# Performance work log

Hardware: AMD Instinct MI355X
Metric: run time of the kernel (lower is better)

The kernel has to match this reference:

```python
import jax, jax.numpy as jnp
import numpy as np

DIM = 1024
HEADS = 16
HEAD_DIM = DIM // HEADS


def setup_inputs() -> dict:
    key = jax.random.key(0)
    k1, k2, k3 = jax.random.split(key, 3)
    x = jax.random.normal(k1, (4, 4096, DIM), dtype=jnp.float32)
    # nn.Linear weights; stored as [out, in] in torch, apply as x @ W.T
    w_qkv = jax.random.normal(k2, (3 * DIM, DIM), dtype=jnp.float32) * (1.0 / np.sqrt(DIM))
    w_out = jax.random.normal(k3, (DIM, DIM), dtype=jnp.float32) * (1.0 / np.sqrt(DIM))
    return {"x": x, "w_qkv": w_qkv, "w_out": w_out}


def _feature_map(t):
    # ELU + 1 (always positive)
    return jax.nn.elu(t) + 1.0


def reference(x, w_qkv, w_out):
    b, n, _ = x.shape
    qkv = x @ w_qkv.T  # [b, n, 3*dim]
    q, k, v = jnp.split(qkv, 3, axis=-1)
    # [b, n, dim] -> [b, h, n, d]
    def to_heads(t):
        return t.reshape(b, n, HEADS, HEAD_DIM).transpose(0, 2, 1, 3)
    q, k, v = to_heads(q), to_heads(k), to_heads(v)
    q = _feature_map(q)
    k = _feature_map(k)
    # KV state: [b, h, d, e]
    kv = jnp.einsum('bhnd,bhne->bhde', k, v)
    out = jnp.einsum('bhnd,bhde->bhne', q, kv)  # [b, h, n, e]
    k_sum = k.sum(axis=2)  # [b, h, d]
    normalizer = jnp.einsum('bhnd,bhd->bhn', q, k_sum)  # [b, h, n]
    out = out / (normalizer[..., None] + 1e-06)
    out = out.transpose(0, 2, 1, 3).reshape(b, n, DIM)
    return out @ w_out.T
```

## Files before the change

### kernel.cpp

```cpp
#include <hip/hip_runtime.h>
#include <hip/hip_bf16.h>
#include <stdint.h>

typedef __attribute__((ext_vector_type(8))) short short8;
typedef __attribute__((ext_vector_type(4))) float f32x4;
typedef __attribute__((ext_vector_type(4))) unsigned short ushort4_t;

#define SEG 16

__device__ __forceinline__ float bf2f(unsigned short u) {
  unsigned int x = ((unsigned int)u) << 16;
  return __uint_as_float(x);
}
__device__ __forceinline__ unsigned short f2bf(float f) {
  unsigned int u = __float_as_uint(f);
  u += 0x7fffu + ((u >> 16) & 1u);
  return (unsigned short)(u >> 16);
}

__device__ __forceinline__ void gload16(const unsigned short* g, unsigned short* l) {
  __builtin_amdgcn_global_load_lds(
      (const __attribute__((address_space(1))) void*)g,
      (__attribute__((address_space(3))) void*)l, 16, 0, 0);
}

__global__ void cast_f32_bf16(const float* __restrict__ in,
                              unsigned short* __restrict__ out, int n4) {
  const int stride = gridDim.x * blockDim.x;
  for (int i = blockIdx.x * blockDim.x + threadIdx.x; i < n4; i += stride) {
    const float4 v = ((const float4*)in)[i];
    ushort4_t o;
    o[0] = f2bf(v.x); o[1] = f2bf(v.y); o[2] = f2bf(v.z); o[3] = f2bf(v.w);
    ((ushort4_t*)out)[i] = o;
  }
}

#define MIDBAR() do { __builtin_amdgcn_sched_barrier(0); __builtin_amdgcn_s_barrier(); } while (0)
#define ENDBAR() do { __builtin_amdgcn_s_barrier(); __builtin_amdgcn_sched_barrier(0); } while (0)

template <typename OutT>
__global__ __launch_bounds__(512, 4) void gemm_v3(
    const unsigned short* __restrict__ A, const unsigned short* __restrict__ Bm,
    OutT* __restrict__ C, int M, int N, int K, int ldc, int fm_cols) {
  __shared__ unsigned short lds[2 * 12288];
  const int tid = threadIdx.x;
  const int lane = tid & 63;
  const int w = tid >> 6;
  const int wr = w >> 1, wc = w & 1;
  const int gx = gridDim.x;
  const int nwg = gx * gridDim.y;
  const int hwid = blockIdx.y * gx + blockIdx.x;
  const int cpx = nwg >> 3;
  const int L = (hwid & 7) * cpx + (hwid >> 3);
  const int bx = L % gx, by = L / gx;
  const size_t arow0 = (size_t)by * 256;
  const size_t bcol0 = (size_t)bx * 128;
  const int nt = K >> 5;

  const int rl = lane >> 2;
  const int sce = (((lane & 3) ^ (rl & 3)) << 3);
  const unsigned short* Ab0 = A + (arow0 + w * 16 + rl) * K + sce;
  const unsigned short* Ab1 = A + (arow0 + 128 + w * 16 + rl) * K + sce;
  const unsigned short* Bb0 = Bm + (bcol0 + w * 16 + rl) * K + sce;

  auto stageA0 = [&](int kt, unsigned short* buf) {
    gload16(Ab0 + ((kt < nt ? kt : kt - nt) << 5), buf + w * 512);
  };
  auto stageA1 = [&](int kt, unsigned short* buf) {
    gload16(Ab1 + ((kt < nt ? kt : kt - nt) << 5), buf + 4096 + w * 512);
  };
  auto stageB = [&](int kt, unsigned short* buf) {
    gload16(Bb0 + ((kt < nt ? kt : kt - nt) << 5), buf + 8192 + w * 512);
  };

  f32x4 acc[4][4] = {};
  const int fr = lane & 15;
  const int kc = lane >> 4;

  auto rdA = [&](const unsigned short* buf, int mm) {
    const int r = wr * 64 + mm * 16 + fr;
    return *(const short8*)&buf[r * 32 + ((kc ^ (r & 3)) << 3)];
  };
  auto rdB = [&](const unsigned short* buf, int nn) {
    const int r = wc * 64 + nn * 16 + fr;
    return *(const short8*)&buf[8192 + r * 32 + ((kc ^ (r & 3)) << 3)];
  };

  stageA0(0, lds); stageA1(0, lds); stageB(0, lds);
  asm volatile("s_waitcnt vmcnt(0)" ::: "memory");
  __builtin_amdgcn_s_barrier();
  __builtin_amdgcn_sched_barrier(0);

  for (int t = 0; t < nt; ++t) {
    unsigned short* cur = lds + (t & 1) * 12288;
    unsigned short* nxt = lds + ((t & 1) ^ 1) * 12288;
    short8 af0, af1, af2, af3, bf0, bf1, bf2, bf3;
    af0 = rdA(cur, 0); af1 = rdA(cur, 1);
    bf0 = rdB(cur, 0); bf1 = rdB(cur, 1);
    stageA0(t + 1, nxt);
    MIDBAR();
    __builtin_amdgcn_s_setprio(1);
    acc[0][0] = __builtin_amdgcn_mfma_f32_16x16x32_bf16(af0, bf0, acc[0][0], 0, 0, 0);
    acc[0][1] = __builtin_amdgcn_mfma_f32_16x16x32_bf16(af0, bf1, acc[0][1], 0, 0, 0);
    acc[1][0] = __builtin_amdgcn_mfma_f32_16x16x32_bf16(af1, bf0, acc[1][0], 0, 0, 0);
    acc[1][1] = __builtin_amdgcn_mfma_f32_16x16x32_bf16(af1, bf1, acc[1][1], 0, 0, 0);
    __builtin_amdgcn_s_setprio(0);
    ENDBAR();
    bf2 = rdB(cur, 2); bf3 = rdB(cur, 3);
    stageA1(t + 1, nxt);
    MIDBAR();
    __builtin_amdgcn_s_setprio(1);
    acc[0][2] = __builtin_amdgcn_mfma_f32_16x16x32_bf16(af0, bf2, acc[0][2], 0, 0, 0);
    acc[0][3] = __builtin_amdgcn_mfma_f32_16x16x32_bf16(af0, bf3, acc[0][3], 0, 0, 0);
    acc[1][2] = __builtin_amdgcn_mfma_f32_16x16x32_bf16(af1, bf2, acc[1][2], 0, 0, 0);
    acc[1][3] = __builtin_amdgcn_mfma_f32_16x16x32_bf16(af1, bf3, acc[1][3], 0, 0, 0);
    __builtin_amdgcn_s_setprio(0);
    ENDBAR();
    af2 = rdA(cur, 2); af3 = rdA(cur, 3);
    stageB(t + 1, nxt);
    MIDBAR();
    __builtin_amdgcn_s_setprio(1);
    acc[2][0] = __builtin_amdgcn_mfma_f32_16x16x32_bf16(af2, bf0, acc[2][0], 0, 0, 0);
    acc[2][1] = __builtin_amdgcn_mfma_f32_16x16x32_bf16(af2, bf1, acc[2][1], 0, 0, 0);
    acc[3][0] = __builtin_amdgcn_mfma_f32_16x16x32_bf16(af3, bf0, acc[3][0], 0, 0, 0);
    acc[3][1] = __builtin_amdgcn_mfma_f32_16x16x32_bf16(af3, bf1, acc[3][1], 0, 0, 0);
    __builtin_amdgcn_s_setprio(0);
    ENDBAR();
    __builtin_amdgcn_s_setprio(1);
    acc[2][2] = __builtin_amdgcn_mfma_f32_16x16x32_bf16(af2, bf2, acc[2][2], 0, 0, 0);
    acc[2][3] = __builtin_amdgcn_mfma_f32_16x16x32_bf16(af2, bf3, acc[2][3], 0, 0, 0);
    acc[3][2] = __builtin_amdgcn_mfma_f32_16x16x32_bf16(af3, bf2, acc[3][2], 0, 0, 0);
    acc[3][3] = __builtin_amdgcn_mfma_f32_16x16x32_bf16(af3, bf3, acc[3][3], 0, 0, 0);
    __builtin_amdgcn_s_setprio(0);
    asm volatile("s_waitcnt vmcnt(0)" ::: "memory");
    __builtin_amdgcn_s_barrier();
    __builtin_amdgcn_sched_barrier(0);
  }

  const int qq = lane >> 4;
#pragma unroll
  for (int m = 0; m < 4; ++m) {
#pragma unroll
    for (int n = 0; n < 4; ++n) {
      const int col = (int)bcol0 + wc * 64 + n * 16 + fr;
      const bool dofm = col < fm_cols;
#pragma unroll
      for (int j = 0; j < 4; ++j) {
        const int row = (int)arow0 + wr * 64 + m * 16 + qq * 4 + j;
        float x = acc[m][n][j];
        if (dofm) x = (x > 0.f) ? x + 1.f : __expf(x);
        if constexpr (sizeof(OutT) == 2) {
          C[(size_t)row * ldc + col] = (OutT)f2bf(x);
        } else {
          C[(size_t)row * ldc + col] = x;
        }
      }
    }
  }
}

__global__ __launch_bounds__(256) void kv_partial(
    const unsigned short* __restrict__ kvmat, float* __restrict__ kvp,
    float* __restrict__ ksp) {
  const int blk = blockIdx.x;
  const int bh = blk >> 4;
  const int seg = blk & (SEG - 1);
  const int b = bh >> 4, h = bh & 15;
  const int rows = 4096 / SEG;
  const size_t row0 = (size_t)b * 4096 + (size_t)seg * rows;
  const unsigned short* kb = kvmat + row0 * 2048 + h * 64;
  const unsigned short* vb = kvmat + row0 * 2048 + 1024 + h * 64;
  __shared__ float kl[32][64];
  __shared__ float vl[32][64];
  const int tid = threadIdx.x;
  const int d0 = (tid >> 4) * 4, e0 = (tid & 15) * 4;
  const int lr = tid >> 3, lc = (tid & 7) * 8;
  float accm[4][4] = {};
  float ksacc[4] = {0.f, 0.f, 0.f, 0.f};

  for (int c = 0; c < rows; c += 32) {
    __syncthreads();
    {
      const short8 k8 = *(const short8*)(kb + (size_t)(c + lr) * 2048 + lc);
      const short8 v8 = *(const short8*)(vb + (size_t)(c + lr) * 2048 + lc);
#pragma unroll
      for (int j = 0; j < 8; ++j) {
        kl[lr][lc + j] = bf2f((unsigned short)k8[j]);
        vl[lr][lc + j] = bf2f((unsigned short)v8[j]);
      }
    }
    __syncthreads();
#pragma unroll
    for (int r = 0; r < 32; ++r) {
      const f32x4 kd = *(const f32x4*)&kl[r][d0];
      const f32x4 ve = *(const f32x4*)&vl[r][e0];
#pragma unroll
      for (int i = 0; i < 4; ++i) {
        ksacc[i] += kd[i];
#pragma unroll
        for (int j = 0; j < 4; ++j) accm[i][j] += kd[i] * ve[j];
      }
    }
  }
  float* kvout = kvp + ((size_t)seg * 64 + bh) * 4096;
#pragma unroll
  for (int i = 0; i < 4; ++i) {
    f32x4 o = {accm[i][0], accm[i][1], accm[i][2], accm[i][3]};
    *(f32x4*)&kvout[(d0 + i) * 64 + e0] = o;
  }
  if ((tid & 15) == 0) {
#pragma unroll
    for (int i = 0; i < 4; ++i)
      ksp[((size_t)seg * 64 + bh) * 64 + d0 + i] = ksacc[i];
  }
}

__global__ void kv_reduce_bf(const float* __restrict__ kvp, const float* __restrict__ ksp,
                             unsigned short* __restrict__ kvb) {
  const int idx = blockIdx.x * 256 + threadIdx.x;
  if (idx >= 64 * 80 * 64) return;
  const int bh = idx / 5120, r = idx % 5120, e = r >> 6, d = r & 63;
  float s = 0.f;
  if (e < 64) {
    for (int g = 0; g < SEG; ++g) s += kvp[((size_t)g * 64 + bh) * 4096 + d * 64 + e];
  } else if (e == 64) {
    for (int g = 0; g < SEG; ++g) s += ksp[((size_t)g * 64 + bh) * 64 + d];
  }
  kvb[idx] = f2bf(s);
}

__global__ __launch_bounds__(256) void attn_mfma(
    const unsigned short* __restrict__ q,
    const unsigned short* __restrict__ kvb,
    unsigned short* __restrict__ att) {
  const int bh = blockIdx.x >> 4;
  const int rt = blockIdx.x & 15;
  const int b = bh >> 4, h = bh & 15;
  __shared__ unsigned short As[2 * 256 * 32];
  __shared__ unsigned short Bs[2 * 80 * 32];
  const int tid = threadIdx.x, lane = tid & 63, wave = tid >> 6;
  const int l4 = lane >> 2;
  const int c8 = (lane & 3) * 8;
  const size_t qrow0 = (size_t)b * 4096 + (size_t)rt * 256;
  const unsigned short* Ab = q + (qrow0 + wave * 64 + l4) * 1024 + h * 64 + c8;
  unsigned short* AsW = As;
#pragma unroll
  for (int ks = 0; ks < 2; ++ks)
#pragma unroll
    for (int i = 0; i < 4; ++i)
      gload16(Ab + (size_t)i * 16 * 1024 + ks * 32,
              AsW + ks * 8192 + wave * 2048 + i * 512);
  for (int c = tid; c < 640; c += 256) {
    const int m0 = c * 8, ks = m0 / 2560, rr = m0 % 2560, e = rr / 32, dk = rr % 32;
    *(short8*)&Bs[m0] = *(const short8*)&kvb[(size_t)bh * 5120 + e * 64 + ks * 32 + dk];
  }
  __syncthreads();

  const int fr = lane & 15, ko = (lane >> 4) * 8;
  short8 af[4][2], bfv[5][2];
#pragma unroll
  for (int m = 0; m < 4; ++m)
#pragma unroll
    for (int ks = 0; ks < 2; ++ks)
      af[m][ks] = *(const short8*)&As[ks * 8192 + (wave * 64 + m * 16 + fr) * 32 + ko];
#pragma unroll
  for (int n = 0; n < 5; ++n)
#pragma unroll
    for (int ks = 0; ks < 2; ++ks)
      bfv[n][ks] = *(const short8*)&Bs[ks * 2560 + (n * 16 + fr) * 32 + ko];
  f32x4 acc[4][5] = {};
#pragma unroll
  for (int m = 0; m < 4; ++m)
#pragma unroll
    for (int n = 0; n < 5; ++n) {
      acc[m][n] = __builtin_amdgcn_mfma_f32_16x16x32_bf16(af[m][0], bfv[n][0], acc[m][n], 0, 0, 0);
      acc[m][n] = __builtin_amdgcn_mfma_f32_16x16x32_bf16(af[m][1], bfv[n][1], acc[m][n], 0, 0, 0);
    }

  const int qq = lane >> 4;
#pragma unroll
  for (int m = 0; m < 4; ++m) {
    f32x4 rnv;
#pragma unroll
    for (int j = 0; j < 4; ++j) {
      const float nv = __shfl(acc[m][4][j], lane & 48);
      rnv[j] = 1.f / (nv + 1e-6f);
    }
    const size_t row = qrow0 + wave * 64 + m * 16 + qq * 4;
#pragma unroll
    for (int n = 0; n < 4; ++n)
#pragma unroll
      for (int j = 0; j < 4; ++j)
        att[(row + j) * 1024 + h * 64 + n * 16 + fr] = f2bf(acc[m][n][j] * rnv[j]);
  }
}

extern "C" void kernel_launch(void* const* d_in, const int* in_sizes, int n_in,
                              void* d_out, int out_size, void* d_ws, size_t ws_size,
                              hipStream_t stream) {
  const float* x = (const float*)d_in[0];
  const float* wqkv = (const float*)d_in[1];
  const float* wout = (const float*)d_in[2];
  float* out = (float*)d_out;

  char* ws = (char*)d_ws;
  size_t off = 0;
  auto alloc = [&](size_t bytes) -> void* {
    void* p = ws + off;
    off += (bytes + 255) & ~(size_t)255;
    return p;
  };
  unsigned short* xbf    = (unsigned short*)alloc((size_t)16384 * 1024 * 2);
  unsigned short* wqkvbf = (unsigned short*)alloc((size_t)3072 * 1024 * 2);
  unsigned short* woutbf = (unsigned short*)alloc((size_t)1024 * 1024 * 2);
  unsigned short* big    = (unsigned short*)alloc((size_t)16384 * 2048 * 2);
  float* kvp = (float*)alloc((size_t)SEG * 64 * 4096 * 4);
  float* ksp = (float*)alloc((size_t)SEG * 64 * 64 * 4);
  unsigned short* kvb = (unsigned short*)alloc((size_t)64 * 80 * 64 * 2);
  unsigned short* qbuf = big;
  unsigned short* att  = big + (size_t)16384 * 1024;

  cast_f32_bf16<<<2048, 256, 0, stream>>>(x, xbf, 16384 * 1024 / 4);
  cast_f32_bf16<<<1024, 256, 0, stream>>>(wqkv, wqkvbf, 3072 * 1024 / 4);
  cast_f32_bf16<<<512, 256, 0, stream>>>(wout, woutbf, 1024 * 1024 / 4);

  gemm_v3<unsigned short><<<dim3(2048 / 128, 16384 / 256), 512, 0, stream>>>(
      xbf, wqkvbf + (size_t)1024 * 1024, big, 16384, 2048, 1024, 2048, 1024);

  kv_partial<<<64 * SEG, 256, 0, stream>>>(big, kvp, ksp);
  kv_reduce_bf<<<1280, 256, 0, stream>>>(kvp, ksp, kvb);

  gemm_v3<unsigned short><<<dim3(1024 / 128, 16384 / 256), 512, 0, stream>>>(
      xbf, wqkvbf, qbuf, 16384, 1024, 1024, 1024, 1024);

  attn_mfma<<<64 * 16, 256, 0, stream>>>(qbuf, kvb, att);

  gemm_v3<float><<<dim3(1024 / 128, 16384 / 256), 512, 0, stream>>>(
      att, woutbf, out, 16384, 1024, 1024, 1024, 0);
}
```

Measured before the change: 266.5 us.

## Triple-buffer GEMM LDS pipeline with two-stage prefetch and single barrier per k-step

The GEMM main loop moves from a double-buffered schedule, with three interleaved barrier phases per k-tile, to a triple-buffered ring. Tiles t+1 and t+2 are in flight while tile t is computed, and the loop waits with vmcnt(3) instead of draining all loads. All fragment reads and 16 MFMAs are now issued together with a single barrier per iteration. The LDS swizzle also gains an extra XOR bit, meant to reduce bank conflicts on the fragment reads. LDS use grows to 72KB per block, which may limit how many blocks fit per CU, and all eight fragments are held in registers at once.

```diff
diff --git a/kernel.cpp b/kernel.cpp
--- a/kernel.cpp
+++ b/kernel.cpp
@@ -35,14 +35,11 @@
   }
 }
 
-#define MIDBAR() do { __builtin_amdgcn_sched_barrier(0); __builtin_amdgcn_s_barrier(); } while (0)
-#define ENDBAR() do { __builtin_amdgcn_s_barrier(); __builtin_amdgcn_sched_barrier(0); } while (0)
-
 template <typename OutT>
-__global__ __launch_bounds__(512, 4) void gemm_v3(
+__global__ __launch_bounds__(512, 4) void gemm_v4(
     const unsigned short* __restrict__ A, const unsigned short* __restrict__ Bm,
     OutT* __restrict__ C, int M, int N, int K, int ldc, int fm_cols) {
-  __shared__ unsigned short lds[2 * 12288];
+  __shared__ unsigned short lds[3 * 12288];
   const int tid = threadIdx.x;
   const int lane = tid & 63;
   const int w = tid >> 6;
@@ -58,19 +55,16 @@
   const int nt = K >> 5;
 
   const int rl = lane >> 2;
-  const int sce = (((lane & 3) ^ (rl & 3)) << 3);
+  const int sce = (((lane & 3) ^ (rl & 3) ^ ((rl >> 2) & 1)) << 3);
   const unsigned short* Ab0 = A + (arow0 + w * 16 + rl) * K + sce;
   const unsigned short* Ab1 = A + (arow0 + 128 + w * 16 + rl) * K + sce;
   const unsigned short* Bb0 = Bm + (bcol0 + w * 16 + rl) * K + sce;
 
-  auto stageA0 = [&](int kt, unsigned short* buf) {
-    gload16(Ab0 + ((kt < nt ? kt : kt - nt) << 5), buf + w * 512);
-  };
-  auto stageA1 = [&](int kt, unsigned short* buf) {
-    gload16(Ab1 + ((kt < nt ? kt : kt - nt) << 5), buf + 4096 + w * 512);
-  };
-  auto stageB = [&](int kt, unsigned short* buf) {
-    gload16(Bb0 + ((kt < nt ? kt : kt - nt) << 5), buf + 8192 + w * 512);
+  auto stage = [&](int kt, unsigned short* buf) {
+    const int k0 = (kt < nt ? kt : kt - nt) << 5;
+    gload16(Ab0 + k0, buf + w * 512);
+    gload16(Ab1 + k0, buf + 4096 + w * 512);
+    gload16(Bb0 + k0, buf + 8192 + w * 512);
   };
 
   f32x4 acc[4][4] = {};
@@ -79,60 +73,44 @@
 
   auto rdA = [&](const unsigned short* buf, int mm) {
     const int r = wr * 64 + mm * 16 + fr;
-    return *(const short8*)&buf[r * 32 + ((kc ^ (r & 3)) << 3)];
+    return *(const short8*)&buf[r * 32 + ((kc ^ (fr & 3) ^ ((fr >> 2) & 1)) << 3)];
   };
   auto rdB = [&](const unsigned short* buf, int nn) {
     const int r = wc * 64 + nn * 16 + fr;
-    return *(const short8*)&buf[8192 + r * 32 + ((kc ^ (r & 3)) << 3)];
+    return *(const short8*)&buf[8192 + r * 32 + ((kc ^ (fr & 3) ^ ((fr >> 2) & 1)) << 3)];
   };
 
-  stageA0(0, lds); stageA1(0, lds); stageB(0, lds);
-  asm volatile("s_waitcnt vmcnt(0)" ::: "memory");
+  stage(0, lds);
+  stage(1, lds + 12288);
+  asm volatile("s_waitcnt vmcnt(3)" ::: "memory");
   __builtin_amdgcn_s_barrier();
   __builtin_amdgcn_sched_barrier(0);
 
   for (int t = 0; t < nt; ++t) {
-    unsigned short* cur = lds + (t & 1) * 12288;
-    unsigned short* nxt = lds + ((t & 1) ^ 1) * 12288;
-    short8 af0, af1, af2, af3, bf0, bf1, bf2, bf3;
-    af0 = rdA(cur, 0); af1 = rdA(cur, 1);
-    bf0 = rdB(cur, 0); bf1 = rdB(cur, 1);
-    stageA0(t + 1, nxt);
-    MIDBAR();
+    const unsigned short* cur = lds + (t % 3) * 12288;
+    unsigned short* nxt = lds + ((t + 2) % 3) * 12288;
+    stage(t + 2, nxt);
+    const short8 af0 = rdA(cur, 0), af1 = rdA(cur, 1), af2 = rdA(cur, 2), af3 = rdA(cur, 3);
+    const short8 bf0 = rdB(cur, 0), bf1 = rdB(cur, 1), bf2 = rdB(cur, 2), bf3 = rdB(cur, 3);
     __builtin_amdgcn_s_setprio(1);
     acc[0][0] = __builtin_amdgcn_mfma_f32_16x16x32_bf16(af0, bf0, acc[0][0], 0, 0, 0);
     acc[0][1] = __builtin_amdgcn_mfma_f32_16x16x32_bf16(af0, bf1, acc[0][1], 0, 0, 0);
     acc[1][0] = __builtin_amdgcn_mfma_f32_16x16x32_bf16(af1, bf0, acc[1][0], 0, 0, 0);
     acc[1][1] = __builtin_amdgcn_mfma_f32_16x16x32_bf16(af1, bf1, acc[1][1], 0, 0, 0);
-    __builtin_amdgcn_s_setprio(0);
-    ENDBAR();
-    bf2 = rdB(cur, 2); bf3 = rdB(cur, 3);
-    stageA1(t + 1, nxt);
-    MIDBAR();
-    __builtin_amdgcn_s_setprio(1);
     acc[0][2] = __builtin_amdgcn_mfma_f32_16x16x32_bf16(af0, bf2, acc[0][2], 0, 0, 0);
     acc[0][3] = __builtin_amdgcn_mfma_f32_16x16x32_bf16(af0, bf3, acc[0][3], 0, 0, 0);
     acc[1][2] = __builtin_amdgcn_mfma_f32_16x16x32_bf16(af1, bf2, acc[1][2], 0, 0, 0);
     acc[1][3] = __builtin_amdgcn_mfma_f32_16x16x32_bf16(af1, bf3, acc[1][3], 0, 0, 0);
-    __builtin_amdgcn_s_setprio(0);
-    ENDBAR();
-    af2 = rdA(cur, 2); af3 = rdA(cur, 3);
-    stageB(t + 1, nxt);
-    MIDBAR();
-    __builtin_amdgcn_s_setprio(1);
     acc[2][0] = __builtin_amdgcn_mfma_f32_16x16x32_bf16(af2, bf0, acc[2][0], 0, 0, 0);
     acc[2][1] = __builtin_amdgcn_mfma_f32_16x16x32_bf16(af2, bf1, acc[2][1], 0, 0, 0);
     acc[3][0] = __builtin_amdgcn_mfma_f32_16x16x32_bf16(af3, bf0, acc[3][0], 0, 0, 0);
     acc[3][1] = __builtin_amdgcn_mfma_f32_16x16x32_bf16(af3, bf1, acc[3][1], 0, 0, 0);
-    __builtin_amdgcn_s_setprio(0);
-    ENDBAR();
-    __builtin_amdgcn_s_setprio(1);
     acc[2][2] = __builtin_amdgcn_mfma_f32_16x16x32_bf16(af2, bf2, acc[2][2], 0, 0, 0);
     acc[2][3] = __builtin_amdgcn_mfma_f32_16x16x32_bf16(af2, bf3, acc[2][3], 0, 0, 0);
     acc[3][2] = __builtin_amdgcn_mfma_f32_16x16x32_bf16(af3, bf2, acc[3][2], 0, 0, 0);
     acc[3][3] = __builtin_amdgcn_mfma_f32_16x16x32_bf16(af3, bf3, acc[3][3], 0, 0, 0);
     __builtin_amdgcn_s_setprio(0);
-    asm volatile("s_waitcnt vmcnt(0)" ::: "memory");
+    asm volatile("s_waitcnt vmcnt(3)" ::: "memory");
     __builtin_amdgcn_s_barrier();
     __builtin_amdgcn_sched_barrier(0);
   }
@@ -324,17 +302,17 @@
   cast_f32_bf16<<<1024, 256, 0, stream>>>(wqkv, wqkvbf, 3072 * 1024 / 4);
   cast_f32_bf16<<<512, 256, 0, stream>>>(wout, woutbf, 1024 * 1024 / 4);
 
-  gemm_v3<unsigned short><<<dim3(2048 / 128, 16384 / 256), 512, 0, stream>>>(
+  gemm_v4<unsigned short><<<dim3(2048 / 128, 16384 / 256), 512, 0, stream>>>(
       xbf, wqkvbf + (size_t)1024 * 1024, big, 16384, 2048, 1024, 2048, 1024);
 
   kv_partial<<<64 * SEG, 256, 0, stream>>>(big, kvp, ksp);
   kv_reduce_bf<<<1280, 256, 0, stream>>>(kvp, ksp, kvb);
 
-  gemm_v3<unsigned short><<<dim3(1024 / 128, 16384 / 256), 512, 0, stream>>>(
+  gemm_v4<unsigned short><<<dim3(1024 / 128, 16384 / 256), 512, 0, stream>>>(
       xbf, wqkvbf, qbuf, 16384, 1024, 1024, 1024, 1024);
 
   attn_mfma<<<64 * 16, 256, 0, stream>>>(qbuf, kvb, att);
 
-  gemm_v3<float><<<dim3(1024 / 128, 16384 / 256), 512, 0, stream>>>(
+  gemm_v4<float><<<dim3(1024 / 128, 16384 / 256), 512, 0, stream>>>(
       att, woutbf, out, 16384, 1024, 1024, 1024, 0);
 }
```

Result: slower. 272.6 us (+2.3%).
